# Optimization experiments

Measured on AMD Instinct MI355X. Metric: run time of the kernel, lower is better.

Reference implementation:

```python
import jax, jax.numpy as jnp
import numpy as np
import math

B, N, E, H = 16, 1024, 512, 8
DH = E // H

def setup_inputs() -> dict:
    key = jax.random.key(0)
    ks = jax.random.split(key, 12)
    inp = {
        "q": jax.random.normal(ks[0], (B, N, E), dtype=jnp.float32),
        "k": jax.random.normal(ks[1], (B, N, E), dtype=jnp.float32),
        "v": jax.random.normal(ks[2], (B, N, E), dtype=jnp.float32),
        "d": jax.random.uniform(ks[3], (B, N, N), dtype=jnp.float32),
        # nn.Linear weights (out, in) with orthogonal-ish init scaled small, zero bias
        "Wq": jax.random.normal(ks[4], (E, E), dtype=jnp.float32) * 0.01,
        "bq": jnp.zeros((E,), dtype=jnp.float32),
        "Wk": jax.random.normal(ks[5], (E, E), dtype=jnp.float32) * 0.01,
        "bk": jnp.zeros((E,), dtype=jnp.float32),
        "Wv": jax.random.normal(ks[6], (E, E), dtype=jnp.float32) * 0.01,
        "bv": jnp.zeros((E,), dtype=jnp.float32),
        "Wp": jax.random.normal(ks[7], (E, E), dtype=jnp.float32) * 0.01,
        "bp": jnp.zeros((E,), dtype=jnp.float32),
    }
    return inp

def _heads(x, W, b):
    # torch Linear: x @ W.T + b, then split heads -> [B, H, N, DH]
    y = jnp.einsum('bne,fe->bnf', x, W) + b
    return y.reshape(x.shape[0], x.shape[1], H, DH).transpose(0, 2, 1, 3)

def reference(q, k, v, d, Wq, bq, Wk, bk, Wv, bv, Wp, bp):
    qh = _heads(q, Wq, bq)                                  # [B,H,N,DH]
    kh = _heads(k, Wk, bk)
    vh = _heads(v, Wv, bv)
    scale = 1.0 / math.sqrt(DH)
    att = jnp.einsum('bhnd,bhmd->bhnm', qh, kh) * scale     # [B,H,N,N]
    db = d[:, None, :, :]                                   # broadcast over heads
    att = jax.nn.softmax(att + db, axis=-1)
    att = att * db                                          # multiplicative distance bias post-softmax
    x = jnp.einsum('bhnm,bhmd->bhnd', att, vh)              # [B,H,N,DH]
    x = x.transpose(0, 2, 1, 3).reshape(q.shape[0], q.shape[1], E)
    return jnp.einsum('bne,fe->bnf', x, Wp) + bp
```

## Files before the change

### kernel.cpp

```cpp
#include <hip/hip_runtime.h>
#include <hip/hip_bf16.h>


#define Bc  16
#define Nc  1024
#define Ec  512
#define Hc  8
#define DHc 64

typedef float  f32x4  __attribute__((ext_vector_type(4)));
typedef int    i32x4  __attribute__((ext_vector_type(4)));
typedef short  s16x4  __attribute__((ext_vector_type(4)));
typedef short  s16x8  __attribute__((ext_vector_type(8)));
typedef __bf16 bf16x8 __attribute__((ext_vector_type(8)));

static __device__ __forceinline__ f32x4 mfma16(s16x8 a, s16x8 b, f32x4 c) {
    return __builtin_amdgcn_mfma_f32_16x16x32_bf16(
        __builtin_bit_cast(bf16x8, a), __builtin_bit_cast(bf16x8, b), c, 0, 0, 0);
}

static __device__ __forceinline__ unsigned short f2bf(float f) {
    return __builtin_bit_cast(unsigned short, __float2bfloat16(f));
}

static __device__ __forceinline__ s16x8 pack_bf16(f32x4 a, f32x4 b) {
    s16x8 r;
    r[0] = (short)f2bf(a[0]); r[1] = (short)f2bf(a[1]);
    r[2] = (short)f2bf(a[2]); r[3] = (short)f2bf(a[3]);
    r[4] = (short)f2bf(b[0]); r[5] = (short)f2bf(b[1]);
    r[6] = (short)f2bf(b[2]); r[7] = (short)f2bf(b[3]);
    return r;
}

static __device__ __forceinline__ void gld16(const void* g, void* l) {
    __builtin_amdgcn_global_load_lds(
        (const __attribute__((address_space(1))) void*)g,
        (__attribute__((address_space(3))) void*)l, 16, 0, 0);
}

static __device__ __forceinline__ void lds_publish_barrier() {
    asm volatile("s_waitcnt lgkmcnt(0)" ::: "memory");
    __builtin_amdgcn_s_barrier();
    asm volatile("" ::: "memory");
}
static __device__ __forceinline__ void plain_barrier() {
    asm volatile("" ::: "memory");
    __builtin_amdgcn_s_barrier();
    asm volatile("" ::: "memory");
}

__global__ __launch_bounds__(256) void wcvt_kernel(
    const float* __restrict__ Wq, const float* __restrict__ Wk,
    const float* __restrict__ Wv, const float* __restrict__ Wp,
    unsigned short* __restrict__ wbf)
{
    const int seg = blockIdx.x >> 7;
    const float* src = seg == 0 ? Wq : (seg == 1 ? Wk : (seg == 2 ? Wv : Wp));
    const int g = (blockIdx.x & 127) * 256 + threadIdx.x;
    const float* p = src + (size_t)g * 8;
    f32x4 a = *(const f32x4*)p, b = *(const f32x4*)(p + 4);
    *(s16x8*)(wbf + (size_t)seg * 262144 + (size_t)g * 8) = pack_bf16(a, b);
}

__global__ __launch_bounds__(256) void proj3_kernel(
    const float* __restrict__ qi, const float* __restrict__ ki,
    const float* __restrict__ vi, const unsigned short* __restrict__ wbf,
    const float* __restrict__ bq, const float* __restrict__ bk,
    const float* __restrict__ bv,
    unsigned short* __restrict__ qo, unsigned short* __restrict__ ko,
    unsigned short* __restrict__ vo)
{
    const int z = blockIdx.z;
    const float* Af = z == 0 ? qi : (z == 1 ? ki : vi);
    const unsigned short* Wb = wbf + (size_t)z * 262144;
    const float* bias = z == 0 ? bq : (z == 1 ? bk : bv);
    unsigned short* out = z == 0 ? qo : (z == 1 ? ko : vo);
    const int mode = (z == 2) ? 1 : 0;

    __shared__ float As_raw[128 * 32];
    __shared__ unsigned short Bsb[128 * 32];

    const int tid = threadIdx.x;
    const int w = tid >> 6, lane = tid & 63;
    const int lr = lane & 15, grp = lane >> 4;
    const int wr = w >> 1, wc = w & 1;
    const int m0 = blockIdx.x * 128, n0 = blockIdx.y * 128;

    f32x4 acc[4][4];
#pragma unroll
    for (int i = 0; i < 4; ++i)
#pragma unroll
        for (int j = 0; j < 4; ++j) acc[i][j] = (f32x4)(0.0f);

    const int h8 = lane >> 3, l8 = lane & 7;
    const int fcol = ((l8 ^ h8) << 2);
    const int h4 = lane >> 2, l4 = lane & 3;
    const int bcol = ((l4 ^ (h4 & 3)) << 3);
    const int o0 = (((grp << 1) ^ (lr & 7)) << 2);
    const int ob = ((grp ^ (lr & 3)) << 3);

    for (int k0 = 0; k0 < Ec; k0 += 32) {
        __syncthreads();
#pragma unroll
        for (int i = 0; i < 4; ++i) {
            const int chunk = i * 4 + w;
            const int row = chunk * 8 + h8;
            gld16(Af + (size_t)(m0 + row) * Ec + k0 + fcol,
                  (char*)As_raw + chunk * 1024 + lane * 16);
        }
#pragma unroll
        for (int i = 0; i < 2; ++i) {
            const int chunk = i * 4 + w;
            const int row = chunk * 16 + h4;
            gld16(Wb + (size_t)(n0 + row) * Ec + k0 + bcol,
                  (char*)Bsb + chunk * 1024 + lane * 16);
        }
        __syncthreads();

        s16x8 afr[4], bfr[4];
#pragma unroll
        for (int mi = 0; mi < 4; ++mi) {
            const float* p = As_raw + (wr * 64 + mi * 16 + lr) * 32;
            afr[mi] = pack_bf16(*(const f32x4*)(p + o0), *(const f32x4*)(p + (o0 ^ 4)));
        }
#pragma unroll
        for (int ni = 0; ni < 4; ++ni)
            bfr[ni] = *(const s16x8*)(Bsb + (wc * 64 + ni * 16 + lr) * 32 + ob);
#pragma unroll
        for (int mi = 0; mi < 4; ++mi)
#pragma unroll
            for (int ni = 0; ni < 4; ++ni)
                acc[mi][ni] = mfma16(afr[mi], bfr[ni], acc[mi][ni]);
    }

#pragma unroll
    for (int mi = 0; mi < 4; ++mi) {
        const int mbase = m0 + wr * 64 + mi * 16 + grp * 4;
#pragma unroll
        for (int ni = 0; ni < 4; ++ni) {
            const int f = n0 + wc * 64 + ni * 16 + lr;
            const float bi = bias[f];
            f32x4 vv = acc[mi][ni];
            const int hh = f >> 6, dh = f & 63;
            if (mode == 0) {
#pragma unroll
                for (int r = 0; r < 4; ++r) {
                    const int m = mbase + r;
                    out[(((size_t)(m >> 10) * Hc + hh) * Nc + (m & (Nc - 1))) * DHc + dh] =
                        f2bf(vv[r] + bi);
                }
            } else {
                const int bb = mbase >> 10, n = mbase & (Nc - 1);
                s16x4 pk;
#pragma unroll
                for (int r = 0; r < 4; ++r) pk[r] = (short)f2bf(vv[r] + bi);
                *(s16x4*)&out[(((size_t)bb * Hc + hh) * DHc + dh) * Nc + n] = pk;
            }
        }
    }
}

__global__ __launch_bounds__(256) void outproj_kernel(
    const unsigned short* __restrict__ Ab, const unsigned short* __restrict__ Wb,
    const float* __restrict__ bias, float* __restrict__ out)
{
    __shared__ unsigned short Asb[128 * 32];
    __shared__ unsigned short Bsb[128 * 32];

    const int tid = threadIdx.x;
    const int w = tid >> 6, lane = tid & 63;
    const int lr = lane & 15, grp = lane >> 4;
    const int wr = w >> 1, wc = w & 1;
    const int m0 = blockIdx.x * 128, n0 = blockIdx.y * 128;

    f32x4 acc[4][4];
#pragma unroll
    for (int i = 0; i < 4; ++i)
#pragma unroll
        for (int j = 0; j < 4; ++j) acc[i][j] = (f32x4)(0.0f);

    const int h4 = lane >> 2, l4 = lane & 3;
    const int bcol = ((l4 ^ (h4 & 3)) << 3);
    const int ob = ((grp ^ (lr & 3)) << 3);

    for (int k0 = 0; k0 < Ec; k0 += 32) {
        __syncthreads();
#pragma unroll
        for (int i = 0; i < 2; ++i) {
            const int chunk = i * 4 + w;
            const int row = chunk * 16 + h4;
            gld16(Ab + (size_t)(m0 + row) * Ec + k0 + bcol,
                  (char*)Asb + chunk * 1024 + lane * 16);
            gld16(Wb + (size_t)(n0 + row) * Ec + k0 + bcol,
                  (char*)Bsb + chunk * 1024 + lane * 16);
        }
        __syncthreads();

        s16x8 afr[4], bfr[4];
#pragma unroll
        for (int mi = 0; mi < 4; ++mi)
            afr[mi] = *(const s16x8*)(Asb + (wr * 64 + mi * 16 + lr) * 32 + ob);
#pragma unroll
        for (int ni = 0; ni < 4; ++ni)
            bfr[ni] = *(const s16x8*)(Bsb + (wc * 64 + ni * 16 + lr) * 32 + ob);
#pragma unroll
        for (int mi = 0; mi < 4; ++mi)
#pragma unroll
            for (int ni = 0; ni < 4; ++ni)
                acc[mi][ni] = mfma16(afr[mi], bfr[ni], acc[mi][ni]);
    }

#pragma unroll
    for (int mi = 0; mi < 4; ++mi) {
        const int mbase = m0 + wr * 64 + mi * 16 + grp * 4;
#pragma unroll
        for (int ni = 0; ni < 4; ++ni) {
            const int f = n0 + wc * 64 + ni * 16 + lr;
            const float bi = bias[f];
            f32x4 vv = acc[mi][ni];
#pragma unroll
            for (int r = 0; r < 4; ++r)
                out[(size_t)(mbase + r) * Ec + f] = vv[r] + bi;
        }
    }
}

__global__ __launch_bounds__(256) void attn_kernel(
    const unsigned short* __restrict__ qh, const unsigned short* __restrict__ kh,
    const unsigned short* __restrict__ vt, const float* __restrict__ dmat,
    unsigned short* __restrict__ xh)
{
    __shared__ unsigned short K_lds[64 * 64];
    __shared__ unsigned short V_lds[64 * 64];
    __shared__ unsigned short P_lds[4][32][72];

    const int lin = blockIdx.x;
    const int swz = ((lin & 7) << 7) | (lin >> 3);
    const int qt = swz & 7, h = (swz >> 3) & 7, b = swz >> 6;

    const int tid = threadIdx.x;
    const int w = tid >> 6, lane = tid & 63;
    const int lr = lane & 15, grp = lane >> 4;
    const int h8 = lane >> 3, l8 = lane & 7;
    const int q0 = qt * 128;
    const int bh = b * Hc + h;
    const int qw = q0 + w * 32;
    const int kofs = grp * 4;
    const int scol = (l8 ^ h8) * 8;
    const float* dbase0 = dmat + ((size_t)b * Nc + qw + lr) * Nc;
    const float* dbase1 = dbase0 + (size_t)16 * Nc;

    const float LOG2E = 1.4426950408889634f;
    const float SC    = 0.125f * LOG2E;
    const float MC    = -4.0f * LOG2E;

    s16x8 bq0[2], bq1[2];
#pragma unroll
    for (int ks = 0; ks < 2; ++ks) {
        bq0[ks] = *reinterpret_cast<const s16x8*>(
            qh + ((size_t)bh * Nc + qw + lr) * DHc + ks * 32 + grp * 8);
        bq1[ks] = *reinterpret_cast<const s16x8*>(
            qh + ((size_t)bh * Nc + qw + 16 + lr) * DHc + ks * 32 + grp * 8);
    }

    f32x4 acc0[4], acc1[4];
#pragma unroll
    for (int c = 0; c < 4; ++c) { acc0[c] = (f32x4)(0.0f); acc1[c] = (f32x4)(0.0f); }
    float lsum0 = 0.f, lsum1 = 0.f;

    const int NT = Nc / 64;
    i32x4 kst[2], vst[2];
#pragma unroll
    for (int i = 0; i < 2; ++i) {
        const int ch = w + i * 4;
        kst[i] = *reinterpret_cast<const i32x4*>(
            kh + ((size_t)bh * Nc + ch * 8 + h8) * DHc + scol);
        vst[i] = *reinterpret_cast<const i32x4*>(
            vt + ((size_t)bh * DHc + ch * 8 + h8) * Nc + scol);
    }
    f32x4 dv0[4], dv1[4];
#pragma unroll
    for (int c = 0; c < 4; ++c) {
        dv0[c] = *reinterpret_cast<const f32x4*>(dbase0 + c * 16 + kofs);
        dv1[c] = *reinterpret_cast<const f32x4*>(dbase1 + c * 16 + kofs);
    }

    for (int kt = 0; kt < NT; ++kt) {
#pragma unroll
        for (int i = 0; i < 2; ++i) {
            const int ch = w + i * 4;
            *reinterpret_cast<i32x4*>((char*)K_lds + ch * 1024 + lane * 16) = kst[i];
            *reinterpret_cast<i32x4*>((char*)V_lds + ch * 1024 + lane * 16) = vst[i];
        }
        if (kt + 1 < NT) {
            const int k1 = (kt + 1) * 64;
#pragma unroll
            for (int i = 0; i < 2; ++i) {
                const int ch = w + i * 4;
                kst[i] = *reinterpret_cast<const i32x4*>(
                    kh + ((size_t)bh * Nc + k1 + ch * 8 + h8) * DHc + scol);
                vst[i] = *reinterpret_cast<const i32x4*>(
                    vt + ((size_t)bh * DHc + ch * 8 + h8) * Nc + k1 + scol);
            }
        }
        lds_publish_barrier();

        f32x4 lgt0[4], lgt1[4];
#pragma unroll
        for (int c = 0; c < 4; ++c) { lgt0[c] = (f32x4)(0.0f); lgt1[c] = (f32x4)(0.0f); }
        __builtin_amdgcn_s_setprio(1);
#pragma unroll
        for (int ks = 0; ks < 2; ++ks) {
#pragma unroll
            for (int c = 0; c < 4; ++c) {
                const int row = c * 16 + lr;
                const int slot = (4 * ks + grp) ^ (lr & 7);
                s16x8 ak = *reinterpret_cast<const s16x8*>(
                    (const char*)K_lds + row * 128 + slot * 16);
                lgt0[c] = mfma16(ak, bq0[ks], lgt0[c]);
                lgt1[c] = mfma16(ak, bq1[ks], lgt1[c]);
            }
        }
        __builtin_amdgcn_s_setprio(0);
#pragma unroll
        for (int c = 0; c < 4; ++c) {
            s16x4 pk0, pk1;
#pragma unroll
            for (int r = 0; r < 4; ++r) {
                const float dl0 = fmaf(dv0[c][r], LOG2E, MC);
                const float p0 = __builtin_amdgcn_exp2f(fmaf(lgt0[c][r], SC, dl0));
                lsum0 += p0;
                pk0[r] = (short)f2bf(p0 * dv0[c][r]);
                const float dl1 = fmaf(dv1[c][r], LOG2E, MC);
                const float p1 = __builtin_amdgcn_exp2f(fmaf(lgt1[c][r], SC, dl1));
                lsum1 += p1;
                pk1[r] = (short)f2bf(p1 * dv1[c][r]);
            }
            *reinterpret_cast<s16x4*>(&P_lds[w][lr][c * 16 + kofs]) = pk0;
            *reinterpret_cast<s16x4*>(&P_lds[w][16 + lr][c * 16 + kofs]) = pk1;
        }
        if (kt + 1 < NT) {
            const int k1 = (kt + 1) * 64;
#pragma unroll
            for (int c = 0; c < 4; ++c) {
                dv0[c] = *reinterpret_cast<const f32x4*>(dbase0 + k1 + c * 16 + kofs);
                dv1[c] = *reinterpret_cast<const f32x4*>(dbase1 + k1 + c * 16 + kofs);
            }
        }
        __builtin_amdgcn_s_setprio(1);
#pragma unroll
        for (int ks = 0; ks < 2; ++ks) {
            s16x8 pa0 = *reinterpret_cast<const s16x8*>(&P_lds[w][lr][ks * 32 + grp * 8]);
            s16x8 pa1 = *reinterpret_cast<const s16x8*>(&P_lds[w][16 + lr][ks * 32 + grp * 8]);
#pragma unroll
            for (int c = 0; c < 4; ++c) {
                const int row = c * 16 + lr;
                const int slot = (4 * ks + grp) ^ (lr & 7);
                s16x8 bv = *reinterpret_cast<const s16x8*>(
                    (const char*)V_lds + row * 128 + slot * 16);
                acc0[c] = mfma16(pa0, bv, acc0[c]);
                acc1[c] = mfma16(pa1, bv, acc1[c]);
            }
        }
        __builtin_amdgcn_s_setprio(0);
        plain_barrier();
    }
    lsum0 += __shfl_xor(lsum0, 16, 64);
    lsum0 += __shfl_xor(lsum0, 32, 64);
    lsum1 += __shfl_xor(lsum1, 16, 64);
    lsum1 += __shfl_xor(lsum1, 32, 64);
    const float invd0 = 1.0f / lsum0, invd1 = 1.0f / lsum1;
    float inv0[4], inv1[4];
#pragma unroll
    for (int r = 0; r < 4; ++r) {
        inv0[r] = __shfl(invd0, grp * 4 + r, 64);
        inv1[r] = __shfl(invd1, grp * 4 + r, 64);
    }
#pragma unroll
    for (int c = 0; c < 4; ++c)
#pragma unroll
        for (int r = 0; r < 4; ++r) {
            xh[((size_t)b * Nc + qw + grp * 4 + r) * Ec + h * DHc + c * 16 + lr] =
                f2bf(acc0[c][r] * inv0[r]);
            xh[((size_t)b * Nc + qw + 16 + grp * 4 + r) * Ec + h * DHc + c * 16 + lr] =
                f2bf(acc1[c][r] * inv1[r]);
        }
}

extern "C" void kernel_launch(void* const* d_in, const int* in_sizes, int n_in,
                              void* d_out, int out_size, void* d_ws, size_t ws_size,
                              hipStream_t stream)
{
    (void)in_sizes; (void)n_in; (void)out_size; (void)ws_size;
    const float* q  = (const float*)d_in[0];
    const float* k  = (const float*)d_in[1];
    const float* v  = (const float*)d_in[2];
    const float* dm = (const float*)d_in[3];
    const float* Wq = (const float*)d_in[4];
    const float* bq = (const float*)d_in[5];
    const float* Wk = (const float*)d_in[6];
    const float* bk = (const float*)d_in[7];
    const float* Wv = (const float*)d_in[8];
    const float* bv = (const float*)d_in[9];
    const float* Wp = (const float*)d_in[10];
    const float* bp = (const float*)d_in[11];
    float* out = (float*)d_out;

    const size_t sz = (size_t)Bc * Hc * Nc * DHc;
    unsigned short* qhb = (unsigned short*)d_ws;
    unsigned short* khb = qhb + sz;
    unsigned short* vtb = khb + sz;
    unsigned short* xhb = vtb + sz;
    unsigned short* wbf = xhb + sz;

    wcvt_kernel<<<dim3(512), dim3(256), 0, stream>>>(Wq, Wk, Wv, Wp, wbf);
    proj3_kernel<<<dim3(Bc * Nc / 128, Ec / 128, 3), dim3(256), 0, stream>>>(
        q, k, v, wbf, bq, bk, bv, qhb, khb, vtb);
    attn_kernel<<<dim3(Bc * Hc * Nc / 128), dim3(256), 0, stream>>>(
        qhb, khb, vtb, dm, xhb);
    outproj_kernel<<<dim3(Bc * Nc / 128, Ec / 128), dim3(256), 0, stream>>>(
        xhb, wbf + (size_t)3 * 262144, bp, out);
}
```

Measured before the change: 158.5 us.

## Double-buffer K/V tiles in LDS to drop one barrier per iteration

The attention kernel now keeps two LDS buffers for K and V. Each iteration writes the next tile into the alternate buffer while computing on the current one, and register prefetch moves two tiles ahead. This removes the trailing barrier, leaving one barrier per key tile, and lets LDS stores overlap compute. The cost is doubled K/V LDS usage, which could reduce occupancy, plus an extra register-staged tile in flight.

```diff
diff --git a/kernel.cpp b/kernel.cpp
--- a/kernel.cpp
+++ b/kernel.cpp
@@ -40,11 +40,6 @@
 
 static __device__ __forceinline__ void lds_publish_barrier() {
     asm volatile("s_waitcnt lgkmcnt(0)" ::: "memory");
-    __builtin_amdgcn_s_barrier();
-    asm volatile("" ::: "memory");
-}
-static __device__ __forceinline__ void plain_barrier() {
-    asm volatile("" ::: "memory");
     __builtin_amdgcn_s_barrier();
     asm volatile("" ::: "memory");
 }
@@ -230,8 +225,8 @@
     const unsigned short* __restrict__ vt, const float* __restrict__ dmat,
     unsigned short* __restrict__ xh)
 {
-    __shared__ unsigned short K_lds[64 * 64];
-    __shared__ unsigned short V_lds[64 * 64];
+    __shared__ unsigned short K_lds[2][64 * 64];
+    __shared__ unsigned short V_lds[2][64 * 64];
     __shared__ unsigned short P_lds[4][32][72];
 
     const int lin = blockIdx.x;
@@ -278,6 +273,20 @@
         vst[i] = *reinterpret_cast<const i32x4*>(
             vt + ((size_t)bh * DHc + ch * 8 + h8) * Nc + scol);
     }
+#pragma unroll
+    for (int i = 0; i < 2; ++i) {
+        const int ch = w + i * 4;
+        *reinterpret_cast<i32x4*>((char*)K_lds[0] + ch * 1024 + lane * 16) = kst[i];
+        *reinterpret_cast<i32x4*>((char*)V_lds[0] + ch * 1024 + lane * 16) = vst[i];
+    }
+#pragma unroll
+    for (int i = 0; i < 2; ++i) {
+        const int ch = w + i * 4;
+        kst[i] = *reinterpret_cast<const i32x4*>(
+            kh + ((size_t)bh * Nc + 64 + ch * 8 + h8) * DHc + scol);
+        vst[i] = *reinterpret_cast<const i32x4*>(
+            vt + ((size_t)bh * DHc + ch * 8 + h8) * Nc + 64 + scol);
+    }
     f32x4 dv0[4], dv1[4];
 #pragma unroll
     for (int c = 0; c < 4; ++c) {
@@ -286,24 +295,27 @@
     }
 
     for (int kt = 0; kt < NT; ++kt) {
-#pragma unroll
-        for (int i = 0; i < 2; ++i) {
-            const int ch = w + i * 4;
-            *reinterpret_cast<i32x4*>((char*)K_lds + ch * 1024 + lane * 16) = kst[i];
-            *reinterpret_cast<i32x4*>((char*)V_lds + ch * 1024 + lane * 16) = vst[i];
-        }
+        const int cur = kt & 1;
+        lds_publish_barrier();
         if (kt + 1 < NT) {
-            const int k1 = (kt + 1) * 64;
+#pragma unroll
+            for (int i = 0; i < 2; ++i) {
+                const int ch = w + i * 4;
+                *reinterpret_cast<i32x4*>((char*)K_lds[cur ^ 1] + ch * 1024 + lane * 16) = kst[i];
+                *reinterpret_cast<i32x4*>((char*)V_lds[cur ^ 1] + ch * 1024 + lane * 16) = vst[i];
+            }
+        }
+        if (kt + 2 < NT) {
+            const int k2 = (kt + 2) * 64;
 #pragma unroll
             for (int i = 0; i < 2; ++i) {
                 const int ch = w + i * 4;
                 kst[i] = *reinterpret_cast<const i32x4*>(
-                    kh + ((size_t)bh * Nc + k1 + ch * 8 + h8) * DHc + scol);
+                    kh + ((size_t)bh * Nc + k2 + ch * 8 + h8) * DHc + scol);
                 vst[i] = *reinterpret_cast<const i32x4*>(
-                    vt + ((size_t)bh * DHc + ch * 8 + h8) * Nc + k1 + scol);
-            }
-        }
-        lds_publish_barrier();
+                    vt + ((size_t)bh * DHc + ch * 8 + h8) * Nc + k2 + scol);
+            }
+        }
 
         f32x4 lgt0[4], lgt1[4];
 #pragma unroll
@@ -316,7 +328,7 @@
                 const int row = c * 16 + lr;
                 const int slot = (4 * ks + grp) ^ (lr & 7);
                 s16x8 ak = *reinterpret_cast<const s16x8*>(
-                    (const char*)K_lds + row * 128 + slot * 16);
+                    (const char*)K_lds[cur] + row * 128 + slot * 16);
                 lgt0[c] = mfma16(ak, bq0[ks], lgt0[c]);
                 lgt1[c] = mfma16(ak, bq1[ks], lgt1[c]);
             }
@@ -357,13 +369,12 @@
                 const int row = c * 16 + lr;
                 const int slot = (4 * ks + grp) ^ (lr & 7);
                 s16x8 bv = *reinterpret_cast<const s16x8*>(
-                    (const char*)V_lds + row * 128 + slot * 16);
+                    (const char*)V_lds[cur] + row * 128 + slot * 16);
                 acc0[c] = mfma16(pa0, bv, acc0[c]);
                 acc1[c] = mfma16(pa1, bv, acc1[c]);
             }
         }
         __builtin_amdgcn_s_setprio(0);
-        plain_barrier();
     }
     lsum0 += __shfl_xor(lsum0, 16, 64);
     lsum0 += __shfl_xor(lsum0, 32, 64);
```

After: 161.0 us. No clear change (+1.6%).
